# Performance work log

Hardware: AMD Instinct MI355X
Metric: run time of the kernel (lower is better)

## Reference

```python
import jax, jax.numpy as jnp
import numpy as np

B, T, D = 2, 2048, 1024
N_HEADS, D_HEAD, WINDOW = 16, 64, 256
SCALE = D_HEAD ** -0.5


def setup_inputs() -> dict:
    key = jax.random.key(0)
    k1, k2, k3 = jax.random.split(key, 3)
    x = jax.random.normal(k1, (B, T, D), dtype=jnp.float32)
    # torch Linear weights are [out_features, in_features], init std=0.02
    w_qkv = jax.random.normal(k2, (3 * N_HEADS * D_HEAD, D), dtype=jnp.float32) * 0.02
    w_out = jax.random.normal(k3, (D, N_HEADS * D_HEAD), dtype=jnp.float32) * 0.02
    return {"x": x, "w_qkv": w_qkv, "w_out": w_out}


def reference(x, w_qkv, w_out):
    b, t, d = x.shape
    qkv = jnp.einsum('btd,ed->bte', x, w_qkv)  # [B,T,3*H*Dh]
    q, k, v = jnp.split(qkv, 3, axis=-1)
    def heads(u):
        return u.reshape(b, t, N_HEADS, D_HEAD).transpose(0, 2, 1, 3)  # [B,H,T,Dh]
    q, k, v = heads(q), heads(k), heads(v)
    scores = jnp.einsum('bhqd,bhkd->bhqk', q, k) * SCALE  # [B,H,T,T]
    pos = jnp.arange(t)
    dist = pos[:, None] - pos[None, :]  # query - key
    allowed = (dist >= 0) & (dist < WINDOW)  # causal sliding window
    neg_inf = jnp.asarray(-jnp.inf, dtype=scores.dtype)
    scores = jnp.where(allowed[None, None], scores, neg_inf)
    attn = jax.nn.softmax(scores, axis=-1)
    out = jnp.einsum('bhqk,bhkd->bhqd', attn, v)  # [B,H,T,Dh]
    out = out.transpose(0, 2, 1, 3).reshape(b, t, N_HEADS * D_HEAD)
    return jnp.einsum('bte,de->btd', out, w_out)
```

## Files before the change

### kernel.cpp

```cpp
#include <hip/hip_runtime.h>
#include <hip/hip_bf16.h>

typedef unsigned short bfu;
typedef __attribute__((ext_vector_type(8))) short short8;
typedef __attribute__((ext_vector_type(4))) float floatx4;
typedef __attribute__((ext_vector_type(2))) __fp16 fp16x2;
typedef __attribute__((ext_vector_type(4))) _Float16 half4v;

#define B_ 2
#define T_ 2048
#define D_ 1024
#define NH 16
#define DH 64
#define WIN 256
#define QKV_COLS 3072
#define NX  (B_ * T_ * D_)
#define NWQ (QKV_COLS * D_)
#define NWO (D_ * D_)

__device__ __forceinline__ bfu f2b_bits(float f) {
  union { __hip_bfloat16 h; bfu u; } cv;
  cv.h = __float2bfloat16(f);
  return cv.u;
}

__device__ __forceinline__ void gl_lds16(const bfu* g, bfu* l) {
  __builtin_amdgcn_global_load_lds(
      (const __attribute__((address_space(1))) unsigned int*)g,
      (__attribute__((address_space(3))) unsigned int*)l, 16, 0, 0);
}

__global__ void cvt3_kernel(const float* __restrict__ x, const float* __restrict__ wq,
                            const float* __restrict__ wo, bfu* __restrict__ out) {
  int i = (blockIdx.x * 256 + threadIdx.x) * 4;
  const float* src;
  int off;
  if (i < NX)            { src = x;  off = 0; }
  else if (i < NX + NWQ) { src = wq; off = NX; }
  else                   { src = wo; off = NX + NWQ; }
  floatx4 v = *(const floatx4*)(src + (i - off));
  out[i + 0] = f2b_bits(v.x);
  out[i + 1] = f2b_bits(v.y);
  out[i + 2] = f2b_bits(v.z);
  out[i + 3] = f2b_bits(v.w);
}

template <int EPI, int TN>
__global__ __launch_bounds__(256) void gemm_bt_kernel(const bfu* __restrict__ A,
                                                      const bfu* __restrict__ Bm,
                                                      void* __restrict__ C,
                                                      int M, int N, int K) {
  constexpr int NJ = TN / 32;
  __shared__ __align__(16) bfu As[128][64];
  __shared__ __align__(16) bfu Bs[TN][64];
  const int tid = threadIdx.x;
  const int wave = tid >> 6, lane = tid & 63;
  const int quad = lane >> 4, cl = lane & 15;
  const int lr = lane >> 3, lg = lane & 7, sg = lg ^ lr;
  const int wm = (wave >> 1) * 64, wn = (wave & 1) * (TN / 2);
  const int m0 = blockIdx.y * 128, n0 = blockIdx.x * TN;

  floatx4 acc[4][NJ] = {};

  for (int k0 = 0; k0 < K; k0 += 64) {
    __syncthreads();
#pragma unroll
    for (int i = 0; i < 4; ++i) {
      const int row = i * 32 + wave * 8;
      gl_lds16(A + (size_t)(m0 + row + lr) * K + k0 + sg * 8, &As[row][0]);
    }
#pragma unroll
    for (int i = 0; i < TN / 32; ++i) {
      const int row = i * 32 + wave * 8;
      gl_lds16(Bm + (size_t)(n0 + row + lr) * K + k0 + sg * 8, &Bs[row][0]);
    }
    __syncthreads();
#pragma unroll
    for (int ks = 0; ks < 2; ++ks) {
      const int gsw = ks * 4 + quad;
      short8 af[4], bfr[NJ];
#pragma unroll
      for (int im = 0; im < 4; ++im)
        af[im] = *(const short8*)(&As[wm + im * 16 + cl][(gsw ^ (cl & 7)) << 3]);
#pragma unroll
      for (int in = 0; in < NJ; ++in)
        bfr[in] = *(const short8*)(&Bs[wn + in * 16 + cl][(gsw ^ (cl & 7)) << 3]);
#pragma unroll
      for (int im = 0; im < 4; ++im)
#pragma unroll
        for (int in = 0; in < NJ; ++in)
          acc[im][in] = __builtin_amdgcn_mfma_f32_16x16x32_bf16(af[im], bfr[in], acc[im][in], 0, 0, 0);
    }
  }
  const float qs = (EPI == 2 && n0 < 1024) ? 0.125f : 1.0f;
  const bool vf16 = (EPI == 2) && (n0 >= 2048);
#pragma unroll
  for (int im = 0; im < 4; ++im) {
#pragma unroll
    for (int r = 0; r < 4; ++r) {
      const size_t row = (size_t)(m0 + wm + im * 16 + quad * 4 + r);
#pragma unroll
      for (int in = 0; in < NJ; ++in) {
        const size_t idx = row * (size_t)N + (n0 + wn + in * 16 + cl);
        const float val = acc[im][in][r];
        if constexpr (EPI == 0) {
          ((float*)C)[idx] = val;
        } else {
          bfu bits;
          if (vf16) { union { _Float16 h; bfu u; } cv; cv.h = (_Float16)val; bits = cv.u; }
          else      { bits = f2b_bits(val * qs); }
          ((bfu*)C)[idx] = bits;
        }
      }
    }
  }
}

__global__ __launch_bounds__(256, 4) void swa_kernel(const bfu* __restrict__ qkv,
                                                     bfu* __restrict__ aout) {
  __shared__ __align__(16) bfu Qs[64][64];
  __shared__ __align__(16) bfu Ks[2][64][64];
  __shared__ __align__(16) bfu Vs[2][64][64];

  const int qt = blockIdx.x, h = blockIdx.y, b = blockIdx.z;
  const int tid = threadIdx.x, wave = tid >> 6, lane = tid & 63;
  const int quad = lane >> 4, cl = lane & 15;
  const int lr = lane >> 3, lg = lane & 7, sg = lg ^ lr;
  const int q0 = qt * 64;
  const bfu* qb = qkv + (size_t)b * T_ * QKV_COLS + h * DH;
  const bfu* kb = qb + 1024;
  const bfu* vb = qb + 2048;

  const int jt0 = (qt >= 4) ? qt - 4 : 0;
  const int njt = qt - jt0 + 1;

  int vrow[2], vcol[2];
#pragma unroll
  for (int i = 0; i < 2; ++i) {
    const int c = tid + i * 256;
    vrow[i] = c >> 3;
    vcol[i] = (c & 7) * 8;
  }

#pragma unroll
  for (int i = 0; i < 2; ++i) {
    const int row = wave * 16 + i * 8;
    gl_lds16(qb + (size_t)(q0 + row + lr) * QKV_COLS + sg * 8, &Qs[row][0]);
    gl_lds16(kb + (size_t)(jt0 * 64 + row + lr) * QKV_COLS + sg * 8, &Ks[0][row][0]);
  }
  {
    union { short8 v; bfu u[8]; } t0[2];
#pragma unroll
    for (int i = 0; i < 2; ++i)
      t0[i].v = *(const short8*)(vb + (size_t)(jt0 * 64 + vrow[i]) * QKV_COLS + vcol[i]);
#pragma unroll
    for (int i = 0; i < 2; ++i)
#pragma unroll
      for (int e = 0; e < 8; ++e) {
        const int d = vcol[i] + e, k = vrow[i];
        const int gp = ((k >> 2) + d + (d >> 3)) & 15;
        Vs[0][d][gp * 4 + (k & 3)] = t0[i].u[e];
      }
  }
  __syncthreads();

  float l_acc = 0.f;
  floatx4 acc[4] = {};
  const int ddc = cl + (cl >> 3);

  for (int it = 0; it < njt; ++it) {
    const int cur = it & 1, nxt = cur ^ 1;
    const int k0 = (jt0 + it) * 64;
    const bool pf = (it + 1 < njt);

    union { short8 v; bfu u[8]; } vp[2];
    if (pf) {
      const int kn = k0 + 64;
#pragma unroll
      for (int i = 0; i < 2; ++i) {
        const int row = wave * 16 + i * 8;
        gl_lds16(kb + (size_t)(kn + row + lr) * QKV_COLS + sg * 8, &Ks[nxt][row][0]);
      }
#pragma unroll
      for (int i = 0; i < 2; ++i)
        vp[i].v = *(const short8*)(vb + (size_t)(kn + vrow[i]) * QKV_COLS + vcol[i]);
    }

    floatx4 s[4] = {};
#pragma unroll
    for (int ks = 0; ks < 2; ++ks) {
      const int col = ((ks * 4 + quad) ^ (cl & 7)) << 3;
      short8 bq = *(const short8*)(&Qs[wave * 16 + cl][col]);
#pragma unroll
      for (int jk = 0; jk < 4; ++jk) {
        short8 ak = *(const short8*)(&Ks[cur][jk * 16 + cl][col]);
        s[jk] = __builtin_amdgcn_mfma_f32_16x16x32_bf16(ak, bq, s[jk], 0, 0, 0);
      }
    }

    const int qg = q0 + wave * 16 + cl;
    half4v af[4];
#pragma unroll
    for (int jk = 0; jk < 4; ++jk) {
      float p[4];
#pragma unroll
      for (int r = 0; r < 4; ++r) {
        const int kg = k0 + jk * 16 + quad * 4 + r;
        const int dist = qg - kg;
        p[r] = (dist >= 0 && dist < WIN) ? __expf(s[jk][r]) : 0.f;
        l_acc += p[r];
      }
      union { fp16x2 h2[2]; half4v h4; } u;
      u.h2[0] = __builtin_amdgcn_cvt_pkrtz(p[0], p[1]);
      u.h2[1] = __builtin_amdgcn_cvt_pkrtz(p[2], p[3]);
      af[jk] = u.h4;
    }

#pragma unroll
    for (int kt = 0; kt < 4; ++kt) {
#pragma unroll
      for (int jd = 0; jd < 4; ++jd) {
        const int d = jd * 16 + cl;
        const int gp = (kt * 4 + quad + ddc + jd * 2) & 15;
        half4v bv = *(const half4v*)(&Vs[cur][d][gp * 4]);
        acc[jd] = __builtin_amdgcn_mfma_f32_16x16x16f16(af[kt], bv, acc[jd], 0, 0, 0);
      }
    }

    if (pf) {
#pragma unroll
      for (int i = 0; i < 2; ++i)
#pragma unroll
        for (int e = 0; e < 8; ++e) {
          const int d = vcol[i] + e, k = vrow[i];
          const int gp = ((k >> 2) + d + (d >> 3)) & 15;
          Vs[nxt][d][gp * 4 + (k & 3)] = vp[i].u[e];
        }
    }
    __syncthreads();
  }

  l_acc += __shfl_xor(l_acc, 16);
  l_acc += __shfl_xor(l_acc, 32);
  const float linv = 1.f / l_acc;
  float lq[4];
#pragma unroll
  for (int r = 0; r < 4; ++r) lq[r] = __shfl(linv, quad * 4 + r);

  bfu* ob = aout + (size_t)b * T_ * D_ + h * DH;
#pragma unroll
  for (int r = 0; r < 4; ++r) {
    const size_t row = (size_t)(q0 + wave * 16 + quad * 4 + r);
#pragma unroll
    for (int jd = 0; jd < 4; ++jd)
      ob[row * D_ + jd * 16 + cl] = f2b_bits(acc[jd][r] * lq[r]);
  }
}

extern "C" void kernel_launch(void* const* d_in, const int* in_sizes, int n_in,
                              void* d_out, int out_size, void* d_ws, size_t ws_size,
                              hipStream_t stream) {
  const float* x     = (const float*)d_in[0];
  const float* w_qkv = (const float*)d_in[1];
  const float* w_out = (const float*)d_in[2];
  float* out = (float*)d_out;
  char* ws = (char*)d_ws;

  bfu* xb    = (bfu*)(ws);
  bfu* wqkvb = (bfu*)(ws + (8ull << 20));
  bfu* woutb = (bfu*)(ws + (14ull << 20));
  bfu* qkvb  = (bfu*)(ws + (16ull << 20));
  bfu* attb  = (bfu*)(ws + (40ull << 20));

  cvt3_kernel<<<(NX + NWQ + NWO) / 1024, 256, 0, stream>>>(x, w_qkv, w_out, xb);

  gemm_bt_kernel<2, 128><<<dim3(QKV_COLS / 128, (B_ * T_) / 128), 256, 0, stream>>>(
      xb, wqkvb, qkvb, B_ * T_, QKV_COLS, D_);

  swa_kernel<<<dim3(T_ / 64, NH, B_), 256, 0, stream>>>(qkvb, attb);

  gemm_bt_kernel<0, 64><<<dim3(D_ / 64, (B_ * T_) / 128), 256, 0, stream>>>(
      attb, woutb, out, B_ * T_, D_, D_);
}
```

Baseline: 154.6 us.

## Widen SWA query tile to 128 rows and skip masked 16-key subtiles

The sliding-window attention kernel now handles 128 queries per block with 512 threads (8 waves), so each K/V tile loaded into shared memory serves twice as many query rows. Each thread moves half as much K/V per tile. Per-wave liveness flags skip the QK MFMAs, exp and PV MFMAs for 16-key subtiles that lie entirely outside the causal window. The trade-off is fewer blocks in the grid, larger blocks per CU, and some wave divergence in the inner loop.

```diff
diff --git a/kernel.cpp b/kernel.cpp
--- a/kernel.cpp
+++ b/kernel.cpp
@@ -116,9 +116,9 @@
   }
 }
 
-__global__ __launch_bounds__(256, 4) void swa_kernel(const bfu* __restrict__ qkv,
+__global__ __launch_bounds__(512, 4) void swa_kernel(const bfu* __restrict__ qkv,
                                                      bfu* __restrict__ aout) {
-  __shared__ __align__(16) bfu Qs[64][64];
+  __shared__ __align__(16) bfu Qs[128][64];
   __shared__ __align__(16) bfu Ks[2][64][64];
   __shared__ __align__(16) bfu Vs[2][64][64];
 
@@ -126,64 +126,57 @@
   const int tid = threadIdx.x, wave = tid >> 6, lane = tid & 63;
   const int quad = lane >> 4, cl = lane & 15;
   const int lr = lane >> 3, lg = lane & 7, sg = lg ^ lr;
-  const int q0 = qt * 64;
+  const int q0 = qt * 128;
   const bfu* qb = qkv + (size_t)b * T_ * QKV_COLS + h * DH;
   const bfu* kb = qb + 1024;
   const bfu* vb = qb + 2048;
 
-  const int jt0 = (qt >= 4) ? qt - 4 : 0;
-  const int njt = qt - jt0 + 1;
-
-  int vrow[2], vcol[2];
-#pragma unroll
-  for (int i = 0; i < 2; ++i) {
-    const int c = tid + i * 256;
-    vrow[i] = c >> 3;
-    vcol[i] = (c & 7) * 8;
-  }
+  const int jt0 = (qt >= 2) ? 2 * qt - 4 : 0;
+  const int njt = (2 * qt + 1) - jt0 + 1;
+
+  const int vrow = tid >> 3;
+  const int vcol = (tid & 7) * 8;
 
 #pragma unroll
   for (int i = 0; i < 2; ++i) {
     const int row = wave * 16 + i * 8;
     gl_lds16(qb + (size_t)(q0 + row + lr) * QKV_COLS + sg * 8, &Qs[row][0]);
-    gl_lds16(kb + (size_t)(jt0 * 64 + row + lr) * QKV_COLS + sg * 8, &Ks[0][row][0]);
-  }
+  }
+  gl_lds16(kb + (size_t)(jt0 * 64 + wave * 8 + lr) * QKV_COLS + sg * 8, &Ks[0][wave * 8][0]);
   {
-    union { short8 v; bfu u[8]; } t0[2];
-#pragma unroll
-    for (int i = 0; i < 2; ++i)
-      t0[i].v = *(const short8*)(vb + (size_t)(jt0 * 64 + vrow[i]) * QKV_COLS + vcol[i]);
-#pragma unroll
-    for (int i = 0; i < 2; ++i)
-#pragma unroll
-      for (int e = 0; e < 8; ++e) {
-        const int d = vcol[i] + e, k = vrow[i];
-        const int gp = ((k >> 2) + d + (d >> 3)) & 15;
-        Vs[0][d][gp * 4 + (k & 3)] = t0[i].u[e];
-      }
+    union { short8 v; bfu u[8]; } t0;
+    t0.v = *(const short8*)(vb + (size_t)(jt0 * 64 + vrow) * QKV_COLS + vcol);
+#pragma unroll
+    for (int e = 0; e < 8; ++e) {
+      const int d = vcol + e;
+      const int gp = ((vrow >> 2) + d + (d >> 3)) & 15;
+      Vs[0][d][gp * 4 + (vrow & 3)] = t0.u[e];
+    }
   }
   __syncthreads();
 
   float l_acc = 0.f;
   floatx4 acc[4] = {};
   const int ddc = cl + (cl >> 3);
+  const int qw0 = q0 + wave * 16;
 
   for (int it = 0; it < njt; ++it) {
     const int cur = it & 1, nxt = cur ^ 1;
     const int k0 = (jt0 + it) * 64;
     const bool pf = (it + 1 < njt);
 
-    union { short8 v; bfu u[8]; } vp[2];
+    union { short8 v; bfu u[8]; } vp;
     if (pf) {
       const int kn = k0 + 64;
-#pragma unroll
-      for (int i = 0; i < 2; ++i) {
-        const int row = wave * 16 + i * 8;
-        gl_lds16(kb + (size_t)(kn + row + lr) * QKV_COLS + sg * 8, &Ks[nxt][row][0]);
-      }
-#pragma unroll
-      for (int i = 0; i < 2; ++i)
-        vp[i].v = *(const short8*)(vb + (size_t)(kn + vrow[i]) * QKV_COLS + vcol[i]);
+      gl_lds16(kb + (size_t)(kn + wave * 8 + lr) * QKV_COLS + sg * 8, &Ks[nxt][wave * 8][0]);
+      vp.v = *(const short8*)(vb + (size_t)(kn + vrow) * QKV_COLS + vcol);
+    }
+
+    bool live[4];
+#pragma unroll
+    for (int jk = 0; jk < 4; ++jk) {
+      const int kg0 = k0 + jk * 16;
+      live[jk] = (qw0 + 15 >= kg0) && (qw0 <= kg0 + 270);
     }
 
     floatx4 s[4] = {};
@@ -192,16 +185,18 @@
       const int col = ((ks * 4 + quad) ^ (cl & 7)) << 3;
       short8 bq = *(const short8*)(&Qs[wave * 16 + cl][col]);
 #pragma unroll
-      for (int jk = 0; jk < 4; ++jk) {
-        short8 ak = *(const short8*)(&Ks[cur][jk * 16 + cl][col]);
-        s[jk] = __builtin_amdgcn_mfma_f32_16x16x32_bf16(ak, bq, s[jk], 0, 0, 0);
-      }
-    }
-
-    const int qg = q0 + wave * 16 + cl;
-    half4v af[4];
+      for (int jk = 0; jk < 4; ++jk)
+        if (live[jk]) {
+          short8 ak = *(const short8*)(&Ks[cur][jk * 16 + cl][col]);
+          s[jk] = __builtin_amdgcn_mfma_f32_16x16x32_bf16(ak, bq, s[jk], 0, 0, 0);
+        }
+    }
+
+    const int qg = qw0 + cl;
+    half4v af[4] = {};
 #pragma unroll
     for (int jk = 0; jk < 4; ++jk) {
+      if (!live[jk]) continue;
       float p[4];
 #pragma unroll
       for (int r = 0; r < 4; ++r) {
@@ -218,6 +213,7 @@
 
 #pragma unroll
     for (int kt = 0; kt < 4; ++kt) {
+      if (!live[kt]) continue;
 #pragma unroll
       for (int jd = 0; jd < 4; ++jd) {
         const int d = jd * 16 + cl;
@@ -229,13 +225,11 @@
 
     if (pf) {
 #pragma unroll
-      for (int i = 0; i < 2; ++i)
-#pragma unroll
-        for (int e = 0; e < 8; ++e) {
-          const int d = vcol[i] + e, k = vrow[i];
-          const int gp = ((k >> 2) + d + (d >> 3)) & 15;
-          Vs[nxt][d][gp * 4 + (k & 3)] = vp[i].u[e];
-        }
+      for (int e = 0; e < 8; ++e) {
+        const int d = vcol + e;
+        const int gp = ((vrow >> 2) + d + (d >> 3)) & 15;
+        Vs[nxt][d][gp * 4 + (vrow & 3)] = vp.u[e];
+      }
     }
     __syncthreads();
   }
@@ -277,7 +271,7 @@
   gemm_bt_kernel<2, 128><<<dim3(QKV_COLS / 128, (B_ * T_) / 128), 256, 0, stream>>>(
       xb, wqkvb, qkvb, B_ * T_, QKV_COLS, D_);
 
-  swa_kernel<<<dim3(T_ / 64, NH, B_), 256, 0, stream>>>(qkvb, attb);
+  swa_kernel<<<dim3(T_ / 128, NH, B_), 512, 0, stream>>>(qkvb, attb);
 
   gemm_bt_kernel<0, 64><<<dim3(D_ / 64, (B_ * T_) / 128), 256, 0, stream>>>(
       attb, woutb, out, B_ * T_, D_, D_);
```

Result: faster. 150.7 us, median of 2 (-2.5%).
